# Kernel optimization log

Measured on AMD Instinct MI355X. Metric: run time of the kernel, lower is better.

Reference implementation:

```python
import jax, jax.numpy as jnp
import numpy as np

N = 512
NODE_IN = 64
NODE_OUT = 64
ED_IN = 32
ED_OUT = 32
STATE = 80  # must satisfy 2*NODE_IN + ED_IN == 2*STATE
SLOPE = 0.1
EPS = 1e-5


def setup_inputs() -> dict:
    key = jax.random.key(0)
    ks = jax.random.split(key, 10)
    def lin(k, out_f, in_f):
        return jax.random.normal(k, (out_f, in_f), jnp.float32) / np.sqrt(in_f).astype(np.float32)
    x = jax.random.normal(ks[0], (N, NODE_IN), jnp.float32)
    edge_attr = jax.random.normal(ks[1], (N * N, ED_IN), jnp.float32)
    mask = jax.random.randint(ks[2], (N * N, 1), 0, 2).astype(jnp.int32)
    return {
        "x": x,
        "edge_attr": edge_attr,
        "mask": mask,
        "W_nu": lin(ks[3], NODE_OUT, NODE_IN),
        "b_nu": jnp.zeros((NODE_OUT,), jnp.float32),
        "W_h2": lin(ks[4], STATE, 2 * STATE),
        "b_h2": jnp.zeros((STATE,), jnp.float32),
        "W_eo": lin(ks[5], ED_OUT, STATE),
        "b_eo": jnp.zeros((ED_OUT,), jnp.float32),
        "e_vec": jax.random.normal(ks[6], (2 * NODE_OUT + ED_OUT,), jnp.float32) * 0.1,
        "bn_n_w": jnp.ones((NODE_OUT,), jnp.float32),
        "bn_n_b": jnp.zeros((NODE_OUT,), jnp.float32),
        "bn_e_w": jnp.ones((ED_OUT,), jnp.float32),
        "bn_e_b": jnp.zeros((ED_OUT,), jnp.float32),
    }


def _lrelu(v):
    return jax.nn.leaky_relu(v, SLOPE)


def _bn(v, w, b):
    # BatchNorm1d, training-mode (batch stats, biased variance)
    mu = v.mean(axis=0)
    var = v.var(axis=0)
    return (v - mu) / jnp.sqrt(var + EPS) * w + b


def reference(x, edge_attr, mask, W_nu, b_nu, W_h2, b_h2, W_eo, b_eo, e_vec,
              bn_n_w, bn_n_b, bn_e_w, bn_e_b):
    n = x.shape[0]
    m = mask.astype(x.dtype)  # [N*N, 1]
    # triplet_e[i*N+j] = [x_i, edge_attr_{ij}, x_j]
    src = jnp.repeat(x, n, axis=0)          # [N*N, NODE_IN]
    dst = jnp.tile(x, (n, 1))               # [N*N, NODE_IN]
    triplet_e = jnp.concatenate([src, edge_attr, dst], axis=-1)  # [N*N, 2*STATE]
    # NOTE: ed_trans_layer / ed_hidden_1 outputs are dead code in the source.
    h = _lrelu(triplet_e @ W_h2.T + b_h2)                 # [N*N, STATE]
    new_edge_attr = _lrelu(h @ W_eo.T + b_eo)             # [N*N, ED_OUT]
    new_edge_attr = new_edge_attr * m
    xn = _lrelu(x @ W_nu.T + b_nu)                        # [N, NODE_OUT]
    triplet_n = jnp.concatenate(
        [jnp.repeat(xn, n, axis=0), new_edge_attr, jnp.tile(xn, (n, 1))], axis=-1
    ).reshape(n, n, 2 * NODE_OUT + ED_OUT)
    scores = _lrelu(jnp.einsum("ijd,d->ij", triplet_n, e_vec))  # [N, N]
    att = jax.nn.softmax(scores, axis=1)
    att = (att.reshape(n * n, 1) * m).reshape(n, n)
    # dropout disabled (deterministic / eval)
    new_x = att @ xn                                       # [N, NODE_OUT]
    new_x = _bn(new_x, bn_n_w, bn_n_b)
    new_edge_attr = _bn(new_edge_attr, bn_e_w, bn_e_b)
    return new_x, new_edge_attr
```

## Files before the change

### kernel.cpp

```cpp
#include <hip/hip_runtime.h>

#define SLOPE 0.1f
#define EPS 1e-5f

typedef __bf16 bf16x8 __attribute__((ext_vector_type(8)));
typedef unsigned short u16x8 __attribute__((ext_vector_type(8)));
typedef float f32x4 __attribute__((ext_vector_type(4)));
typedef unsigned u32x4 __attribute__((ext_vector_type(4)));

#define WS_ESC 0
#define WS_ESH 32
#define WS_A 64
#define WS_B 576
#define WS_XN 1088
#define WS_NEWX 33856
#define WS_P1B 66624
#define WS_SC 107584
#define WS_PART 369728
#define WSH_WB 804992
#define WSH_WB2 810112
#define WSH_WO 812672
#define WSH_XB 815744
#define WSH_NE 848512

__device__ __forceinline__ float lrelu(float v) { return v > 0.f ? v : SLOPE * v; }
__device__ __forceinline__ unsigned short f2bf(float f) {
  unsigned x = __float_as_uint(f);
  return (unsigned short)((x + 0x7fffu + ((x >> 16) & 1u)) >> 16);
}
__device__ __forceinline__ float bf2f(unsigned short u) {
  return __uint_as_float(((unsigned)u) << 16);
}

__global__ void __launch_bounds__(256) k1(const float* __restrict__ x,
                                          const float* __restrict__ W_nu,
                                          const float* __restrict__ b_nu,
                                          const float* __restrict__ W_h2,
                                          const float* __restrict__ b_h2,
                                          const float* __restrict__ W_eo,
                                          const float* __restrict__ ev,
                                          float* ws) {
  int blk = blockIdx.x;
  int tid = threadIdx.x;
  unsigned short* wsh = (unsigned short*)ws;
  if (blk < 128) {
    __shared__ float wlds[64 * 65];
#pragma unroll
    for (int it = 0; it < 16; it++) {
      int idx = it * 256 + tid;
      wlds[(idx >> 6) * 65 + (idx & 63)] = W_nu[idx];
    }
    int gid = blk * 256 + tid;
    wsh[WSH_XB + gid] = f2bf(x[gid]);
    ws[WS_PART + gid] = 0.f;
    if (gid < 5120) {
      int c = gid / 2560, r = gid - c * 2560;
      int t = r >> 9, l = (r >> 3) & 63, jj = r & 7;
      int n = t * 16 + (l & 15);
      int k = (l >> 4) * 8 + jj + c * 32;
      wsh[WSH_WB + gid] = f2bf(W_h2[n * 160 + 64 + k]);
    } else if (gid < 7680) {
      int idx = gid - 5120;
      int t = idx >> 9, l = (idx >> 3) & 63, jj = idx & 7;
      int n = t * 16 + (l & 15);
      int k = (l >> 4) * 8 + jj;
      wsh[WSH_WB2 + idx] = f2bf(W_h2[n * 160 + 128 + k]);
    } else if (gid < 10752) {
      int idx = gid - 7680;
      int t2 = idx / 1536, r2 = idx - t2 * 1536;
      int s = r2 >> 9, l = (r2 >> 3) & 63, jj = r2 & 7;
      int n = t2 * 16 + (l & 15);
      int k = s * 32 + (l >> 4) * 8 + jj;
      wsh[WSH_WO + idx] = (k < 80) ? f2bf(W_eo[n * 80 + k]) : (unsigned short)0;
    }
    __syncthreads();
    int i = blk * 4 + (tid >> 6);
    int c = tid & 63;
    float acc = b_nu[c];
    const float* xr = x + i * 64;
#pragma unroll 8
    for (int k = 0; k < 64; k++) acc += xr[k] * wlds[c * 65 + k];
    float xnv = lrelu(acc);
    ws[WS_XN + i * 64 + c] = xnv;
    float va = xnv * ev[c];
    float vb = xnv * ev[96 + c];
#pragma unroll
    for (int off = 32; off >= 1; off >>= 1) {
      va += __shfl_xor(va, off, 64);
      vb += __shfl_xor(vb, off, 64);
    }
    if (c == 0) { ws[WS_A + i] = va; ws[WS_B + i] = vb; }
  } else {
    int b2 = blk - 128;
    int bm = b2 & 7, bn = b2 >> 3;
    int wave = tid >> 6, lane = tid & 63;
    int c16 = lane & 15, q = lane >> 4;
    int n = bn * 16 + c16;
    const float* wrow = W_h2 + n * 160;
    int mrow = bm * 64 + wave * 16 + c16;
    bf16x8 bfr[2], afr[2];
#pragma unroll
    for (int ks = 0; ks < 2; ks++) {
      const float* bs = wrow + ks * 32 + q * 8;
      const float* as = x + mrow * 64 + ks * 32 + q * 8;
      u16x8 ub, ua;
#pragma unroll
      for (int jj = 0; jj < 8; jj++) { ub[jj] = f2bf(bs[jj]); ua[jj] = f2bf(as[jj]); }
      bfr[ks] = __builtin_bit_cast(bf16x8, ub);
      afr[ks] = __builtin_bit_cast(bf16x8, ua);
    }
    float bias = b_h2[n];
    f32x4 acc = {bias, bias, bias, bias};
    acc = __builtin_amdgcn_mfma_f32_16x16x32_bf16(afr[0], bfr[0], acc, 0, 0, 0);
    acc = __builtin_amdgcn_mfma_f32_16x16x32_bf16(afr[1], bfr[1], acc, 0, 0, 0);
#pragma unroll
    for (int r = 0; r < 4; r++) {
      int mm = bm * 64 + wave * 16 + q * 4 + r;
      ws[WS_P1B + mm * 80 + n] = acc[r];
    }
  }
}

__global__ void __launch_bounds__(256) k2(const float* __restrict__ ea,
                                          const int* __restrict__ mask,
                                          const float* __restrict__ b_eo,
                                          const float* __restrict__ ev,
                                          float* ws) {
  __shared__ unsigned short wlds[10752];
  __shared__ unsigned short ht[64 * 104];
  __shared__ float p1s[80];
  __shared__ float wred[2][4][32];
  int tid = threadIdx.x;
  int w = tid >> 6, lane = tid & 63;
  int c16 = lane & 15, q = lane >> 4;
  int blk = blockIdx.x;
  int i = blk >> 1, j0 = (blk & 1) << 8;
  const unsigned short* wsh = (const unsigned short*)ws;
  unsigned* ne32 = (unsigned*)((unsigned short*)ws + WSH_NE);

#pragma unroll
  for (int it = 0; it < 6; it++) {
    int idx = it * 256 + tid;
    if (idx < 1344) *(u16x8*)&wlds[idx * 8] = *(const u16x8*)(wsh + WSH_WB + idx * 8);
  }
  if (tid < 80) p1s[tid] = ws[WS_P1B + i * 80 + tid];
  float beo0 = b_eo[c16], beo1 = b_eo[16 + c16];
  float eve0 = ev[64 + c16], eve1 = ev[80 + c16];
  float a_i = ws[WS_A + i];
  __syncthreads();

  float scs0 = 0.f, scss0 = 0.f, scs1 = 0.f, scss1 = 0.f;

#pragma unroll 2
  for (int h = 0; h < 4; h++) {
    int jb = j0 + h * 64 + w * 16;

    const float* src = ea + (i * 512 + jb + c16) * 32 + q * 8;
    f32x4 e0 = *(const f32x4*)src;
    f32x4 e1 = *(const f32x4*)(src + 4);
    u16x8 ue;
#pragma unroll
    for (int jj = 0; jj < 4; jj++) { ue[jj] = f2bf(e0[jj]); ue[4 + jj] = f2bf(e1[jj]); }
    bf16x8 af0 = __builtin_bit_cast(bf16x8, ue);
    bf16x8 af1 = __builtin_bit_cast(
        bf16x8, *(const u16x8*)(wsh + WSH_XB + (jb + c16) * 64 + q * 8));
    bf16x8 af2 = __builtin_bit_cast(
        bf16x8, *(const u16x8*)(wsh + WSH_XB + (jb + c16) * 64 + 32 + q * 8));
    int4 mk = *(const int4*)(mask + i * 512 + jb + q * 4);
    int mkv[4];
    mkv[0] = mk.x; mkv[1] = mk.y; mkv[2] = mk.z; mkv[3] = mk.w;

    f32x4 acc[5];
#pragma unroll
    for (int t = 0; t < 5; t++) {
      float p1v = p1s[t * 16 + c16];
      acc[t] = {p1v, p1v, p1v, p1v};
    }
#pragma unroll
    for (int t = 0; t < 5; t++) {
      bf16x8 wb = __builtin_bit_cast(bf16x8, *(const u16x8*)&wlds[t * 512 + lane * 8]);
      acc[t] = __builtin_amdgcn_mfma_f32_16x16x32_bf16(af0, wb, acc[t], 0, 0, 0);
    }
#pragma unroll
    for (int t = 0; t < 5; t++) {
      bf16x8 wb =
          __builtin_bit_cast(bf16x8, *(const u16x8*)&wlds[2560 + t * 512 + lane * 8]);
      acc[t] = __builtin_amdgcn_mfma_f32_16x16x32_bf16(af1, wb, acc[t], 0, 0, 0);
    }
#pragma unroll
    for (int t = 0; t < 5; t++) {
      bf16x8 wb =
          __builtin_bit_cast(bf16x8, *(const u16x8*)&wlds[5120 + t * 512 + lane * 8]);
      acc[t] = __builtin_amdgcn_mfma_f32_16x16x32_bf16(af2, wb, acc[t], 0, 0, 0);
    }
#pragma unroll
    for (int t = 0; t < 5; t++)
#pragma unroll
      for (int r = 0; r < 4; r++)
        ht[(w * 16 + q * 4 + r) * 104 + t * 16 + c16] = f2bf(lrelu(acc[t][r]));

    f32x4 acc2[2] = {{0.f, 0.f, 0.f, 0.f}, {0.f, 0.f, 0.f, 0.f}};
    int hrow = w * 16 + c16;
#pragma unroll
    for (int s = 0; s < 3; s++) {
      int kk = s * 32 + q * 8;
      u16x8 hb = {0, 0, 0, 0, 0, 0, 0, 0};
      if (kk < 80) hb = *(const u16x8*)&ht[hrow * 104 + kk];
      bf16x8 ha = __builtin_bit_cast(bf16x8, hb);
      bf16x8 wo0 =
          __builtin_bit_cast(bf16x8, *(const u16x8*)&wlds[7680 + s * 512 + lane * 8]);
      bf16x8 wo1 = __builtin_bit_cast(
          bf16x8, *(const u16x8*)&wlds[7680 + 1536 + s * 512 + lane * 8]);
      acc2[0] = __builtin_amdgcn_mfma_f32_16x16x32_bf16(ha, wo0, acc2[0], 0, 0, 0);
      acc2[1] = __builtin_amdgcn_mfma_f32_16x16x32_bf16(ha, wo1, acc2[1], 0, 0, 0);
    }

    float se[4];
#pragma unroll
    for (int r = 0; r < 4; r++) {
      int m = i * 512 + jb + q * 4 + r;
      float mf = mkv[r] ? 1.f : 0.f;
      float v0 = lrelu(acc2[0][r] + beo0) * mf;
      float v1 = lrelu(acc2[1][r] + beo1) * mf;
      scs0 += v0; scss0 += v0 * v0;
      scs1 += v1; scss1 += v1 * v1;
      ne32[m * 16 + c16] = (unsigned)f2bf(v0) | ((unsigned)f2bf(v1) << 16);
      float s = v0 * eve0 + v1 * eve1;
#pragma unroll
      for (int off = 8; off >= 1; off >>= 1) s += __shfl_xor(s, off, 64);
      se[r] = s;
    }
    if (c16 < 4) {
      int j = jb + q * 4 + c16;
      float s = (c16 == 0) ? se[0] : (c16 == 1) ? se[1] : (c16 == 2) ? se[2] : se[3];
      ws[WS_SC + i * 512 + j] = lrelu(a_i + ws[WS_B + j] + s);
    }
  }

  scs0 += __shfl_xor(scs0, 16, 64); scs0 += __shfl_xor(scs0, 32, 64);
  scss0 += __shfl_xor(scss0, 16, 64); scss0 += __shfl_xor(scss0, 32, 64);
  scs1 += __shfl_xor(scs1, 16, 64); scs1 += __shfl_xor(scs1, 32, 64);
  scss1 += __shfl_xor(scss1, 16, 64); scss1 += __shfl_xor(scss1, 32, 64);
  if (q == 0) {
    wred[0][w][c16] = scs0; wred[0][w][16 + c16] = scs1;
    wred[1][w][c16] = scss0; wred[1][w][16 + c16] = scss1;
  }
  __syncthreads();
  if (tid < 64) {
    int half = tid >> 5, col = tid & 31;
    float v = wred[half][0][col] + wred[half][1][col] + wred[half][2][col] +
              wred[half][3][col];
    atomicAdd(&ws[WS_PART + i * 64 + tid], v);
  }
}

__global__ void __launch_bounds__(512) k3(const int* __restrict__ mask,
                                          const float* __restrict__ bn_e_w,
                                          const float* __restrict__ bn_e_b,
                                          float* ws) {
  __shared__ float att[512];
  __shared__ float red[8];
  __shared__ float nx[8][64];
  int i = blockIdx.x, tid = threadIdx.x;
  int wave = tid >> 6, lane = tid & 63;
  if (i == 512) {
    int g = tid >> 6, c = tid & 63;
    float a = 0.f;
    for (int s = g; s < 512; s += 8) a += ws[WS_PART + s * 64 + c];
    nx[g][c] = a;
    __syncthreads();
    if (tid < 64) {
      float t = 0.f;
#pragma unroll
      for (int g2 = 0; g2 < 8; g2++) t += nx[g2][tid];
      att[tid] = t;
    }
    __syncthreads();
    if (tid < 32) {
      float mean = att[tid] * (1.f / 262144.f);
      float var = att[tid + 32] * (1.f / 262144.f) - mean * mean;
      float s = bn_e_w[tid] * rsqrtf(fmaxf(var, 0.f) + EPS);
      ws[WS_ESC + tid] = s;
      ws[WS_ESH + tid] = bn_e_b[tid] - mean * s;
    }
    return;
  }
  float p = __expf(ws[WS_SC + i * 512 + tid]);
  float sm = p;
#pragma unroll
  for (int off = 32; off >= 1; off >>= 1) sm += __shfl_xor(sm, off, 64);
  if (lane == 0) red[wave] = sm;
  __syncthreads();
  float tot = red[0] + red[1] + red[2] + red[3] + red[4] + red[5] + red[6] + red[7];
  att[tid] = p * (1.f / tot) * (mask[i * 512 + tid] ? 1.f : 0.f);
  __syncthreads();
  int c = lane;
  const float* xn = ws + WS_XN;
  float accv = 0.f;
#pragma unroll 4
  for (int u = 0; u < 64; u++) {
    int j = wave * 64 + u;
    accv += att[j] * xn[j * 64 + c];
  }
  nx[wave][c] = accv;
  __syncthreads();
  if (tid < 64) {
    float s = 0.f;
#pragma unroll
    for (int w = 0; w < 8; w++) s += nx[w][tid];
    ws[WS_NEWX + i * 64 + tid] = s;
  }
}

__global__ void __launch_bounds__(256) k5(const float* __restrict__ bn_n_w,
                                          const float* __restrict__ bn_n_b,
                                          const float* __restrict__ ws,
                                          float* __restrict__ out) {
  int blk = blockIdx.x, tid = threadIdx.x;
  if (blk < 8) {
    __shared__ float s1[4][64], s2[4][64], scl[64], sh[64];
    int c = tid & 63, g = tid >> 6;
    float a = 0.f, b = 0.f;
#pragma unroll 4
    for (int u = 0; u < 128; u++) {
      float v = ws[WS_NEWX + (g * 128 + u) * 64 + c];
      a += v;
      b += v * v;
    }
    s1[g][c] = a;
    s2[g][c] = b;
    __syncthreads();
    if (tid < 64) {
      float sum = s1[0][tid] + s1[1][tid] + s1[2][tid] + s1[3][tid];
      float ssq = s2[0][tid] + s2[1][tid] + s2[2][tid] + s2[3][tid];
      float mean = sum * (1.f / 512.f);
      float var = ssq * (1.f / 512.f) - mean * mean;
      float s = bn_n_w[tid] * rsqrtf(fmaxf(var, 0.f) + EPS);
      scl[tid] = s;
      sh[tid] = bn_n_b[tid] - mean * s;
    }
    __syncthreads();
#pragma unroll 4
    for (int u = 0; u < 16; u++) {
      int idx = blk * 4096 + u * 256 + tid;
      int c2 = idx & 63;
      out[idx] = ws[WS_NEWX + idx] * scl[c2] + sh[c2];
    }
  } else {
    const unsigned* ne32 = (const unsigned*)((const unsigned short*)ws + WSH_NE);
    int b4 = ((blk - 8) * 256 + tid) * 4;
    u32x4 raw = *(const u32x4*)(ne32 + b4);
    int e32 = (b4 >> 4) * 32;
    int cb = b4 & 15;
    f32x4 esc0 = *(const f32x4*)(ws + WS_ESC + cb);
    f32x4 esc1 = *(const f32x4*)(ws + WS_ESC + 16 + cb);
    f32x4 esh0 = *(const f32x4*)(ws + WS_ESH + cb);
    f32x4 esh1 = *(const f32x4*)(ws + WS_ESH + 16 + cb);
    f32x4 lo, hi;
#pragma unroll
    for (int u = 0; u < 4; u++) {
      lo[u] = bf2f((unsigned short)(raw[u] & 0xffffu)) * esc0[u] + esh0[u];
      hi[u] = bf2f((unsigned short)(raw[u] >> 16)) * esc1[u] + esh1[u];
    }
    float* oe = out + 32768;
    *(f32x4*)(oe + e32 + cb) = lo;
    *(f32x4*)(oe + e32 + 16 + cb) = hi;
  }
}

extern "C" void kernel_launch(void* const* d_in, const int* in_sizes, int n_in,
                              void* d_out, int out_size, void* d_ws, size_t ws_size,
                              hipStream_t stream) {
  const float* x = (const float*)d_in[0];
  const float* ea = (const float*)d_in[1];
  const int* mask = (const int*)d_in[2];
  const float* Wnu = (const float*)d_in[3];
  const float* bnu = (const float*)d_in[4];
  const float* Wh2 = (const float*)d_in[5];
  const float* bh2 = (const float*)d_in[6];
  const float* Weo = (const float*)d_in[7];
  const float* beo = (const float*)d_in[8];
  const float* ev = (const float*)d_in[9];
  const float* bnw = (const float*)d_in[10];
  const float* bnb = (const float*)d_in[11];
  const float* bew = (const float*)d_in[12];
  const float* beb = (const float*)d_in[13];
  float* ws = (float*)d_ws;
  float* out = (float*)d_out;

  k1<<<168, 256, 0, stream>>>(x, Wnu, bnu, Wh2, bh2, Weo, ev, ws);
  k2<<<1024, 256, 0, stream>>>(ea, mask, beo, ev, ws);
  k3<<<513, 512, 0, stream>>>(mask, bew, beb, ws);
  k5<<<4104, 256, 0, stream>>>(bnw, bnb, ws, out);
}
```

Measured before the change: 165.0 us.

## Fuse row softmax and attention aggregation into edge kernel, one block per row

The edge kernel now runs one 512-thread block per source node i covering the whole row, so it can keep the score row in shared memory. It then does the softmax, mask, and att @ xn product in place, removing the global score round-trip and the separate per-row kernel. Per-row BN partial sums are written directly instead of via atomics, so the zeroing in k1 is dropped. The BN-stat reduction becomes a single-block kernel. The cost is half as many blocks in k2 and more shared memory per block, which may reduce occupancy.

```diff
diff --git a/kernel.cpp b/kernel.cpp
--- a/kernel.cpp
+++ b/kernel.cpp
@@ -52,7 +52,6 @@
     }
     int gid = blk * 256 + tid;
     wsh[WSH_XB + gid] = f2bf(x[gid]);
-    ws[WS_PART + gid] = 0.f;
     if (gid < 5120) {
       int c = gid / 2560, r = gid - c * 2560;
       int t = r >> 9, l = (r >> 3) & 63, jj = r & 7;
@@ -121,26 +120,28 @@
   }
 }
 
-__global__ void __launch_bounds__(256) k2(const float* __restrict__ ea,
+__global__ void __launch_bounds__(512) k2(const float* __restrict__ ea,
                                           const int* __restrict__ mask,
                                           const float* __restrict__ b_eo,
                                           const float* __restrict__ ev,
                                           float* ws) {
   __shared__ unsigned short wlds[10752];
-  __shared__ unsigned short ht[64 * 104];
+  __shared__ unsigned short ht[128 * 104];
   __shared__ float p1s[80];
-  __shared__ float wred[2][4][32];
+  __shared__ float s_row[512];
+  __shared__ float red[8];
+  __shared__ float nx[8][64];
+  __shared__ float wred[2][8][32];
   int tid = threadIdx.x;
   int w = tid >> 6, lane = tid & 63;
   int c16 = lane & 15, q = lane >> 4;
-  int blk = blockIdx.x;
-  int i = blk >> 1, j0 = (blk & 1) << 8;
+  int i = blockIdx.x;
   const unsigned short* wsh = (const unsigned short*)ws;
   unsigned* ne32 = (unsigned*)((unsigned short*)ws + WSH_NE);
 
 #pragma unroll
-  for (int it = 0; it < 6; it++) {
-    int idx = it * 256 + tid;
+  for (int it = 0; it < 3; it++) {
+    int idx = it * 512 + tid;
     if (idx < 1344) *(u16x8*)&wlds[idx * 8] = *(const u16x8*)(wsh + WSH_WB + idx * 8);
   }
   if (tid < 80) p1s[tid] = ws[WS_P1B + i * 80 + tid];
@@ -151,17 +152,20 @@
 
   float scs0 = 0.f, scss0 = 0.f, scs1 = 0.f, scss1 = 0.f;
 
-#pragma unroll 2
+#pragma unroll
   for (int h = 0; h < 4; h++) {
-    int jb = j0 + h * 64 + w * 16;
-
-    const float* src = ea + (i * 512 + jb + c16) * 32 + q * 8;
-    f32x4 e0 = *(const f32x4*)src;
-    f32x4 e1 = *(const f32x4*)(src + 4);
-    u16x8 ue;
-#pragma unroll
-    for (int jj = 0; jj < 4; jj++) { ue[jj] = f2bf(e0[jj]); ue[4 + jj] = f2bf(e1[jj]); }
-    bf16x8 af0 = __builtin_bit_cast(bf16x8, ue);
+    int jb = w * 64 + h * 16;
+
+    bf16x8 af0;
+    {
+      const float* src = ea + (i * 512 + jb + c16) * 32 + q * 8;
+      f32x4 e0 = *(const f32x4*)src;
+      f32x4 e1 = *(const f32x4*)(src + 4);
+      u16x8 u;
+#pragma unroll
+      for (int jj = 0; jj < 4; jj++) { u[jj] = f2bf(e0[jj]); u[4 + jj] = f2bf(e1[jj]); }
+      af0 = __builtin_bit_cast(bf16x8, u);
+    }
     bf16x8 af1 = __builtin_bit_cast(
         bf16x8, *(const u16x8*)(wsh + WSH_XB + (jb + c16) * 64 + q * 8));
     bf16x8 af2 = __builtin_bit_cast(
@@ -233,7 +237,7 @@
     if (c16 < 4) {
       int j = jb + q * 4 + c16;
       float s = (c16 == 0) ? se[0] : (c16 == 1) ? se[1] : (c16 == 2) ? se[2] : se[3];
-      ws[WS_SC + i * 512 + j] = lrelu(a_i + ws[WS_B + j] + s);
+      s_row[j] = lrelu(a_i + ws[WS_B + j] + s);
     }
   }
 
@@ -246,69 +250,64 @@
     wred[1][w][c16] = scss0; wred[1][w][16 + c16] = scss1;
   }
   __syncthreads();
-  if (tid < 64) {
-    int half = tid >> 5, col = tid & 31;
-    float v = wred[half][0][col] + wred[half][1][col] + wred[half][2][col] +
-              wred[half][3][col];
-    atomicAdd(&ws[WS_PART + i * 64 + tid], v);
-  }
-}
-
-__global__ void __launch_bounds__(512) k3(const int* __restrict__ mask,
-                                          const float* __restrict__ bn_e_w,
-                                          const float* __restrict__ bn_e_b,
-                                          float* ws) {
-  __shared__ float att[512];
-  __shared__ float red[8];
-  __shared__ float nx[8][64];
-  int i = blockIdx.x, tid = threadIdx.x;
-  int wave = tid >> 6, lane = tid & 63;
-  if (i == 512) {
-    int g = tid >> 6, c = tid & 63;
-    float a = 0.f;
-    for (int s = g; s < 512; s += 8) a += ws[WS_PART + s * 64 + c];
-    nx[g][c] = a;
-    __syncthreads();
-    if (tid < 64) {
-      float t = 0.f;
-#pragma unroll
-      for (int g2 = 0; g2 < 8; g2++) t += nx[g2][tid];
-      att[tid] = t;
-    }
-    __syncthreads();
-    if (tid < 32) {
-      float mean = att[tid] * (1.f / 262144.f);
-      float var = att[tid + 32] * (1.f / 262144.f) - mean * mean;
-      float s = bn_e_w[tid] * rsqrtf(fmaxf(var, 0.f) + EPS);
-      ws[WS_ESC + tid] = s;
-      ws[WS_ESH + tid] = bn_e_b[tid] - mean * s;
-    }
-    return;
-  }
-  float p = __expf(ws[WS_SC + i * 512 + tid]);
+
+  float p = __expf(s_row[tid]);
   float sm = p;
 #pragma unroll
   for (int off = 32; off >= 1; off >>= 1) sm += __shfl_xor(sm, off, 64);
-  if (lane == 0) red[wave] = sm;
+  if (lane == 0) red[w] = sm;
   __syncthreads();
   float tot = red[0] + red[1] + red[2] + red[3] + red[4] + red[5] + red[6] + red[7];
-  att[tid] = p * (1.f / tot) * (mask[i * 512 + tid] ? 1.f : 0.f);
-  __syncthreads();
-  int c = lane;
+  float attv = p * (1.f / tot) * (mask[i * 512 + tid] ? 1.f : 0.f);
+  s_row[tid] = attv;
+  __syncthreads();
+
   const float* xn = ws + WS_XN;
   float accv = 0.f;
 #pragma unroll 4
   for (int u = 0; u < 64; u++) {
-    int j = wave * 64 + u;
-    accv += att[j] * xn[j * 64 + c];
-  }
-  nx[wave][c] = accv;
+    int j = w * 64 + u;
+    accv += s_row[j] * xn[j * 64 + lane];
+  }
+  nx[w][lane] = accv;
   __syncthreads();
   if (tid < 64) {
     float s = 0.f;
 #pragma unroll
-    for (int w = 0; w < 8; w++) s += nx[w][tid];
+    for (int w2 = 0; w2 < 8; w2++) s += nx[w2][tid];
     ws[WS_NEWX + i * 64 + tid] = s;
+    int half = tid >> 5, col = tid & 31;
+    float v = 0.f;
+#pragma unroll
+    for (int w2 = 0; w2 < 8; w2++) v += wred[half][w2][col];
+    ws[WS_PART + i * 64 + tid] = v;
+  }
+}
+
+__global__ void __launch_bounds__(512) k3(const float* __restrict__ bn_e_w,
+                                          const float* __restrict__ bn_e_b,
+                                          float* ws) {
+  __shared__ float nx[8][64];
+  __shared__ float col[64];
+  int tid = threadIdx.x;
+  int w = tid >> 6, lane = tid & 63;
+  float a = 0.f;
+  for (int s = w; s < 512; s += 8) a += ws[WS_PART + s * 64 + lane];
+  nx[w][lane] = a;
+  __syncthreads();
+  if (tid < 64) {
+    float t = 0.f;
+#pragma unroll
+    for (int g2 = 0; g2 < 8; g2++) t += nx[g2][tid];
+    col[tid] = t;
+  }
+  __syncthreads();
+  if (tid < 32) {
+    float mean = col[tid] * (1.f / 262144.f);
+    float var = col[tid + 32] * (1.f / 262144.f) - mean * mean;
+    float s = bn_e_w[tid] * rsqrtf(fmaxf(var, 0.f) + EPS);
+    ws[WS_ESC + tid] = s;
+    ws[WS_ESH + tid] = bn_e_b[tid] - mean * s;
   }
 }
 
@@ -389,7 +388,7 @@
   float* out = (float*)d_out;
 
   k1<<<168, 256, 0, stream>>>(x, Wnu, bnu, Wh2, bh2, Weo, ev, ws);
-  k2<<<1024, 256, 0, stream>>>(ea, mask, beo, ev, ws);
-  k3<<<513, 512, 0, stream>>>(mask, bew, beb, ws);
+  k2<<<512, 512, 0, stream>>>(ea, mask, beo, ev, ws);
+  k3<<<1, 512, 0, stream>>>(bew, beb, ws);
   k5<<<4104, 256, 0, stream>>>(bnw, bnb, ws, out);
 }
```

Result: faster. 159.8 us (-3.2%).
